# Performance work log

Hardware: AMD Instinct MI355X
Metric: run time of the kernel (lower is better)

## Reference

```python
import jax, jax.numpy as jnp
import numpy as np

NUM_BINS = 63          # len(bins); num_embeddings = NUM_BINS + 1
EMB_DIM = 64
B, F = 8192, 64


def setup_inputs() -> dict:
    key = jax.random.key(0)
    kx, kw = jax.random.split(key)
    bins = jnp.asarray(np.linspace(-3.1, 3.1, NUM_BINS), dtype=jnp.float32)
    neg_inf = jnp.array([-jnp.inf], dtype=jnp.float32)
    pos_inf = jnp.array([jnp.inf], dtype=jnp.float32)
    low = jnp.concatenate([neg_inf, bins])    # [K]
    high = jnp.concatenate([bins, pos_inf])   # [K]
    x = jax.random.normal(kx, (B, F), dtype=jnp.float32)
    weight = jax.random.normal(kw, (NUM_BINS + 1, EMB_DIM), dtype=jnp.float32) * 0.02
    return {"x": x, "low": low, "high": high, "weight": weight}


def reference(x, low, high, weight):
    # x: [B,F], low/high: [K], weight: [K,D]
    K = weight.shape[0]
    arange = jnp.arange(K)
    # bucket membership mask (same broadcasted compare as torch)
    s = (x[..., None] > low) & (x[..., None] <= high)      # [B,F,K] bool
    index = jnp.argmax(s, axis=-1)                          # [B,F] first True
    diff = jnp.abs(index[..., None] - arange)               # [B,F,K]
    scale = 1.0 / (diff + 1).astype(weight.dtype)           # mode='linear'
    # distance-weighted sum over all embeddings: [B,F,K] @ [K,D] -> [B,F,D]
    return jnp.einsum('bfk,kd->bfd', scale, weight)
```

## Files before the change

### kernel.cpp

```cpp
#include <hip/hip_runtime.h>

#define NEMB 64
#define DIM  64
#define NBINS 63

__global__ __launch_bounds__(64) void build_table_kernel(
    const float* __restrict__ weight, float* __restrict__ T) {
    const int i = blockIdx.x;
    const int d = threadIdx.x;
    float acc = 0.0f;
    #pragma unroll
    for (int k = 0; k < NEMB; ++k) {
        int diff = i - k;
        diff = diff < 0 ? -diff : diff;
        acc += weight[k * DIM + d] * (1.0f / (float)(diff + 1));
    }
    T[i * DIM + d] = acc;
}

__global__ __launch_bounds__(256) void emb_gather_kernel(
    const float* __restrict__ x,
    const float* __restrict__ low,
    const float* __restrict__ T,
    float* __restrict__ out,
    int n_rows) {
    __shared__ float4 Tlds[NEMB * 16];
    __shared__ float  bins_lds[NBINS];
    __shared__ int    idx_lds[256];

    const int t = threadIdx.x;

    const float4* T4 = reinterpret_cast<const float4*>(T);
    #pragma unroll
    for (int i = 0; i < 4; ++i)
        Tlds[t + 256 * i] = T4[t + 256 * i];
    if (t < NBINS) bins_lds[t] = low[t + 1];
    __syncthreads();

    const int base = blockIdx.x * 256;

    {
        const int row = base + t;
        float xv = (row < n_rows) ? x[row] : 0.0f;
        int c = 0;
        if (xv > bins_lds[c + 31]) c += 32;
        if (xv > bins_lds[c + 15]) c += 16;
        if (xv > bins_lds[c + 7])  c += 8;
        if (xv > bins_lds[c + 3])  c += 4;
        if (xv > bins_lds[c + 1])  c += 2;
        if (xv > bins_lds[c])      c += 1;
        idx_lds[t] = c;
    }
    __syncthreads();

    const int sub   = t >> 4;
    const int lane4 = t & 15;
    float4* out4 = reinterpret_cast<float4*>(out);
    #pragma unroll
    for (int it = 0; it < 16; ++it) {
        const int r    = it * 16 + sub;
        const int grow = base + r;
        if (grow < n_rows) {
            const float4 v = Tlds[idx_lds[r] * 16 + lane4];
            out4[grow * 16 + lane4] = v;
        }
    }
}

extern "C" void kernel_launch(void* const* d_in, const int* in_sizes, int n_in,
                              void* d_out, int out_size, void* d_ws, size_t ws_size,
                              hipStream_t stream) {
    const float* x      = (const float*)d_in[0];
    const float* low    = (const float*)d_in[1];
    const float* weight = (const float*)d_in[3];
    float* out = (float*)d_out;
    float* T   = (float*)d_ws;

    const int n_rows = in_sizes[0];

    build_table_kernel<<<NEMB, DIM, 0, stream>>>(weight, T);

    const int blocks = (n_rows + 255) / 256;
    emb_gather_kernel<<<blocks, 256, 0, stream>>>(x, low, T, out, n_rows);
}
```

Before: 145.3 us.

## Gather table rows from global/L2 instead of LDS and use nontemporal output stores

Drops the per-block copy of the 16KB precomputed table into shared memory and instead reads table rows straight from global memory, where they should stay resident in cache. Output writes become nontemporal stores so the large streaming output does not evict useful cache lines. The table-build kernel is relaunched as 16 blocks of 256 threads instead of 64 blocks of 64. Removing the LDS staging saves per-block load work and shared memory, which may raise occupancy, at the cost of scattered cache-level gathers in place of LDS reads.

```diff
diff --git a/kernel.cpp b/kernel.cpp
--- a/kernel.cpp
+++ b/kernel.cpp
@@ -4,10 +4,13 @@
 #define DIM  64
 #define NBINS 63
 
-__global__ __launch_bounds__(64) void build_table_kernel(
+typedef float f32x4 __attribute__((ext_vector_type(4)));
+
+__global__ __launch_bounds__(256) void build_table_kernel(
     const float* __restrict__ weight, float* __restrict__ T) {
-    const int i = blockIdx.x;
-    const int d = threadIdx.x;
+    const int e = blockIdx.x * 256 + threadIdx.x;
+    const int i = e >> 6;
+    const int d = e & 63;
     float acc = 0.0f;
     #pragma unroll
     for (int k = 0; k < NEMB; ++k) {
@@ -15,25 +18,19 @@
         diff = diff < 0 ? -diff : diff;
         acc += weight[k * DIM + d] * (1.0f / (float)(diff + 1));
     }
-    T[i * DIM + d] = acc;
+    T[e] = acc;
 }
 
 __global__ __launch_bounds__(256) void emb_gather_kernel(
     const float* __restrict__ x,
     const float* __restrict__ low,
-    const float* __restrict__ T,
-    float* __restrict__ out,
+    const f32x4* __restrict__ T4,
+    f32x4* __restrict__ out4,
     int n_rows) {
-    __shared__ float4 Tlds[NEMB * 16];
-    __shared__ float  bins_lds[NBINS];
-    __shared__ int    idx_lds[256];
+    __shared__ float bins_lds[NBINS];
+    __shared__ int   idx_lds[256];
 
     const int t = threadIdx.x;
-
-    const float4* T4 = reinterpret_cast<const float4*>(T);
-    #pragma unroll
-    for (int i = 0; i < 4; ++i)
-        Tlds[t + 256 * i] = T4[t + 256 * i];
     if (t < NBINS) bins_lds[t] = low[t + 1];
     __syncthreads();
 
@@ -55,14 +52,18 @@
 
     const int sub   = t >> 4;
     const int lane4 = t & 15;
-    float4* out4 = reinterpret_cast<float4*>(out);
+
+    int myidx[16];
+    #pragma unroll
+    for (int it = 0; it < 16; ++it)
+        myidx[it] = idx_lds[it * 16 + sub];
+
     #pragma unroll
     for (int it = 0; it < 16; ++it) {
-        const int r    = it * 16 + sub;
-        const int grow = base + r;
+        const int grow = base + it * 16 + sub;
         if (grow < n_rows) {
-            const float4 v = Tlds[idx_lds[r] * 16 + lane4];
-            out4[grow * 16 + lane4] = v;
+            const f32x4 v = T4[myidx[it] * 16 + lane4];
+            __builtin_nontemporal_store(v, &out4[grow * 16 + lane4]);
         }
     }
 }
@@ -78,8 +79,9 @@
 
     const int n_rows = in_sizes[0];
 
-    build_table_kernel<<<NEMB, DIM, 0, stream>>>(weight, T);
+    build_table_kernel<<<16, 256, 0, stream>>>(weight, T);
 
     const int blocks = (n_rows + 255) / 256;
-    emb_gather_kernel<<<blocks, 256, 0, stream>>>(x, low, T, out, n_rows);
+    emb_gather_kernel<<<blocks, 256, 0, stream>>>(
+        x, low, (const f32x4*)T, (f32x4*)out, n_rows);
 }
```

Result: slower. 152.1 us (+4.6%).
